# Kernel tuning notes

Measured on AMD Instinct MI355X. Metric: run time of the kernel, lower is better.

The kernel has to match this reference:

```python
import jax, jax.numpy as jnp
import numpy as np

B, D_IN, M, D_MEM = 65536, 64, 2048, 64


def setup_inputs() -> dict:
    key = jax.random.key(0)
    k = jax.random.split(key, 5)
    glorot = lambda kk, shape: jax.random.uniform(
        kk, shape, jnp.float32,
        -jnp.sqrt(6.0 / (shape[0] + shape[1])), jnp.sqrt(6.0 / (shape[0] + shape[1])))
    return {
        "inputs": jax.random.normal(k[0], (B, D_IN), jnp.float32),
        "W_att": glorot(k[1], (D_IN, M)),
        "b_att": jnp.zeros((M,), jnp.float32),
        "W_write": glorot(k[2], (D_IN, D_MEM)),
        "b_write": jnp.zeros((D_MEM,), jnp.float32),
        "memory": glorot(k[3], (M, D_MEM)),
        "update_gate": jnp.full((M,), 0.5, jnp.float32),
    }


def reference(inputs, W_att, b_att, W_write, b_write, memory, update_gate):
    # Read attention: Dense(memory_size, softmax) -> [B, M]
    read_attention = jax.nn.softmax(inputs @ W_att + b_att, axis=-1)
    # Read: [B, M] @ [M, Dm] -> [B, Dm]
    read_vector = read_attention @ memory
    # Write candidate: Dense(memory_dim, tanh) -> [B, Dm]
    candidate_write = jnp.tanh(inputs @ W_write + b_write)
    aggregated_write = jnp.mean(candidate_write, axis=0)[None, :]  # [1, Dm]
    write_attention = jnp.mean(read_attention, axis=0)             # [M]
    update_weights = (write_attention * update_gate)[:, None]      # [M, 1]
    # Gated in-place memory update (returned as new state)
    new_memory = memory * (1.0 - update_weights) + update_weights * aggregated_write
    return read_vector, new_memory
```

## Files before the change

kernel.cpp:

```cpp
#include <hip/hip_runtime.h>
#include <hip/hip_bf16.h>

typedef unsigned int   u32;
typedef unsigned short u16;

typedef __bf16 bf16x8 __attribute__((ext_vector_type(8)));
typedef float  f32x4  __attribute__((ext_vector_type(4)));
typedef u32    u32x4  __attribute__((ext_vector_type(4)));

union Frag { u32x4 u; bf16x8 b; };

#define MFMA16 __builtin_amdgcn_mfma_f32_16x16x32_bf16

#define B_ROWS 65536
#define D_IN   64
#define M_SZ   2048
#define D_MEM  64

#define WT_OFF      0
#define MEMT_OFF    262144
#define WWT_OFF     524288
#define CSF_OFF     532480
#define AGF_OFF     540672
#define CSP_OFF     540928
#define AGP_OFF     8929536
#define WS_REQUIRED 9191680

#define L2E 1.4426950408889634f

__device__ __forceinline__ float bf2f(u16 h) { return __uint_as_float(((u32)h) << 16); }
__device__ __forceinline__ u16 f2bf(float f) {
    u32 u = __float_as_uint(f);
    return (u16)((u + 0x7FFFu + ((u >> 16) & 1u)) >> 16);
}
__device__ __forceinline__ u16 f2bf_fast(float f) {
    return (u16)((__float_as_uint(f) + 0x8000u) >> 16);
}
#if defined(__has_builtin) && __has_builtin(__builtin_amdgcn_exp2f)
__device__ __forceinline__ float exp2fast(float x) { return __builtin_amdgcn_exp2f(x); }
#else
__device__ __forceinline__ float exp2fast(float x) { return __expf(x * 0.6931471805599453f); }
#endif
__device__ __forceinline__ float tanh_fast(float x) {
    const float e = exp2fast(x * (2.0f * L2E));
    return 1.0f - 2.0f * __builtin_amdgcn_rcpf(e + 1.0f);
}
__device__ __forceinline__ bool detect_bf16(const void* ug) {
    return ((const u32*)ug)[0] == 0x3F003F00u;
}
__device__ __forceinline__ float load_elem(const void* p, size_t i, bool isbf) {
    return isbf ? bf2f(((const u16*)p)[i]) : ((const float*)p)[i];
}

__global__ void __launch_bounds__(256)
prep_kernel(const void* Watt, const void* mem_in, const void* Wwr, const void* ug,
            u16* Wt, u16* memT, u16* Wwt, float* CSF)
{
    const bool isbf = detect_bf16(ug);
    const int b = blockIdx.x;
    const int t = threadIdx.x;
    if (b == 65) {
        for (int i = t; i < 2112; i += 256) CSF[i] = 0.f;
        return;
    }
    __shared__ u16 tile[64][65];
    const void* src; u16* dst; int R, C, rb, cb;
    if (b < 32)      { src = Watt;   dst = Wt;   R = 64;   C = 2048; rb = 0;           cb = b * 64; }
    else if (b < 64) { src = mem_in; dst = memT; R = 2048; C = 64;   rb = (b-32) * 64; cb = 0;      }
    else             { src = Wwr;    dst = Wwt;  R = 64;   C = 64;   rb = 0;           cb = 0;      }

#pragma unroll
    for (int j = 0; j < 16; ++j) {
        int e = j * 256 + t;
        int r = e >> 6, c = e & 63;
        float v = load_elem(src, (size_t)(rb + r) * C + cb + c, isbf);
        tile[r][c] = f2bf(v);
    }
    __syncthreads();
#pragma unroll
    for (int j = 0; j < 16; ++j) {
        int e = j * 256 + t;
        int c2 = e >> 6, r2 = e & 63;
        dst[(size_t)(cb + c2) * R + rb + r2] = tile[r2][c2];
    }
}

__global__ void __launch_bounds__(256, 2)
main_kernel(const void* x_in, const void* batt_in, const void* bwrite_in,
            const u16* __restrict__ Wt, const u16* __restrict__ memT,
            const u16* __restrict__ Wwt, const void* ug,
            float* CSF, float* AGF, u16* cs_part, u16* ag_part,
            int use_part, void* out)
{
    const bool isbf = detect_bf16(ug);
    const int tid = threadIdx.x;
    const int lane = tid & 63, wave = tid >> 6;
    const int quad = lane >> 4, l4 = lane & 15;
    const int rowbase = blockIdx.x * 128;
    const int wrow = blockIdx.x * 4 + wave;

    __shared__ __align__(16) u16 WtL[2][64][72];
    __shared__ __align__(16) u16 MeL[2][64][72];
    __shared__ __align__(16) u16 P[4][32][72];
    __shared__ float battL[2048];

    {
        const int i0 = tid * 8;
#pragma unroll
        for (int j = 0; j < 8; ++j)
            battL[i0 + j] = load_elem(batt_in, i0 + j, isbf) * L2E;
    }

    const int srow = tid >> 2, sg = (tid & 3) * 16;
    auto stageWt = [&](int c, int b) {
        const u16* g = Wt + ((size_t)c * 64 + srow) * 64 + sg;
        u32x4 v0 = *(const u32x4*)g;
        u32x4 v1 = *(const u32x4*)(g + 8);
        *(u32x4*)&WtL[b][srow][sg]     = v0;
        *(u32x4*)&WtL[b][srow][sg + 8] = v1;
    };
    auto stageMe = [&](int c, int b) {
        const u16* g = memT + (size_t)srow * 2048 + c * 64 + sg;
        u32x4 v0 = *(const u32x4*)g;
        u32x4 v1 = *(const u32x4*)(g + 8);
        *(u32x4*)&MeL[b][srow][sg]     = v0;
        *(u32x4*)&MeL[b][srow][sg + 8] = v1;
    };

    Frag a[2][2];
#pragma unroll
    for (int rg = 0; rg < 2; ++rg) {
        const int arow = rowbase + wave * 32 + rg * 16 + l4;
        if (isbf) {
            const u16* xp = (const u16*)x_in + (size_t)arow * 64 + quad * 8;
            a[rg][0].u = *(const u32x4*)xp;
            a[rg][1].u = *(const u32x4*)(xp + 32);
        } else {
            const float* xp = (const float*)x_in + (size_t)arow * 64 + quad * 8;
#pragma unroll
            for (int j = 0; j < 8; ++j) {
                ((u16*)&a[rg][0])[j] = f2bf(xp[j]);
                ((u16*)&a[rg][1])[j] = f2bf(xp[32 + j]);
            }
        }
    }
    const f32x4 zf = {0.f, 0.f, 0.f, 0.f};

    stageWt(0, 0);

    float agout = 0.f;
    {
        f32x4 accW[4][2];
#pragma unroll
        for (int t = 0; t < 4; ++t) {
            const u16* bp = Wwt + (size_t)(t * 16 + l4) * 64 + quad * 8;
            Frag b0, b1; b0.u = *(const u32x4*)bp; b1.u = *(const u32x4*)(bp + 32);
#pragma unroll
            for (int rg = 0; rg < 2; ++rg) {
                accW[t][rg] = MFMA16(a[rg][0].b, b0.b, zf, 0, 0, 0);
                accW[t][rg] = MFMA16(a[rg][1].b, b1.b, accW[t][rg], 0, 0, 0);
            }
        }
#pragma unroll
        for (int t = 0; t < 4; ++t) {
            const float bw = load_elem(bwrite_in, t * 16 + l4, isbf);
            float s = 0.f;
#pragma unroll
            for (int rg = 0; rg < 2; ++rg)
#pragma unroll
                for (int i = 0; i < 4; ++i) s += tanh_fast(accW[t][rg][i] + bw);
            s += __shfl_xor(s, 16, 64);
            s += __shfl_xor(s, 32, 64);
            if (quad == t) agout = s;
        }
    }
    if (use_part) ag_part[wrow * 64 + lane] = f2bf(agout);
    else          atomicAdd(&AGF[lane], agout);

    __syncthreads();

    float lr[2][4] = {{0.f,0.f,0.f,0.f},{0.f,0.f,0.f,0.f}};
    for (int c = 0; c < 32; ++c) {
        const int buf = c & 1;
        if (c < 31) stageWt(c + 1, buf ^ 1);
        const int mbase = c * 64;
        Frag wb0[4], wb1[4]; float bl[4];
#pragma unroll
        for (int t = 0; t < 4; ++t) {
            wb0[t].u = *(const u32x4*)&WtL[buf][t * 16 + l4][quad * 8];
            wb1[t].u = *(const u32x4*)&WtL[buf][t * 16 + l4][32 + quad * 8];
            bl[t] = battL[mbase + t * 16 + l4];
        }
#pragma unroll
        for (int t = 0; t < 4; ++t)
#pragma unroll
            for (int rg = 0; rg < 2; ++rg) {
                f32x4 acc = MFMA16(a[rg][0].b, wb0[t].b, zf, 0, 0, 0);
                acc = MFMA16(a[rg][1].b, wb1[t].b, acc, 0, 0, 0);
#pragma unroll
                for (int i = 0; i < 4; ++i)
                    lr[rg][i] += exp2fast(fmaf(acc[i], L2E, bl[t]));
            }
        __syncthreads();
    }
#pragma unroll
    for (int rg = 0; rg < 2; ++rg)
#pragma unroll
        for (int i = 0; i < 4; ++i) {
            float v = lr[rg][i];
            v += __shfl_xor(v, 1, 64); v += __shfl_xor(v, 2, 64);
            v += __shfl_xor(v, 4, 64); v += __shfl_xor(v, 8, 64);
            lr[rg][i] = 1.f / v;
        }

    f32x4 oacc[2][4] = {{zf,zf,zf,zf},{zf,zf,zf,zf}};
    stageWt(0, 0); stageMe(0, 0);
    __syncthreads();
    for (int c = 0; c < 32; ++c) {
        const int buf = c & 1;
        if (c < 31) { stageWt(c + 1, buf ^ 1); stageMe(c + 1, buf ^ 1); }
        const int mbase = c * 64;
        Frag wb0[4], wb1[4], mb0[4], mb1[4]; float bl[4];
#pragma unroll
        for (int t = 0; t < 4; ++t) {
            wb0[t].u = *(const u32x4*)&WtL[buf][t * 16 + l4][quad * 8];
            wb1[t].u = *(const u32x4*)&WtL[buf][t * 16 + l4][32 + quad * 8];
            bl[t] = battL[mbase + t * 16 + l4];
            mb0[t].u = *(const u32x4*)&MeL[buf][t * 16 + l4][quad * 8];
            mb1[t].u = *(const u32x4*)&MeL[buf][t * 16 + l4][32 + quad * 8];
        }
        float cst[4];
#pragma unroll
        for (int t = 0; t < 4; ++t) {
            float cs = 0.f;
#pragma unroll
            for (int rg = 0; rg < 2; ++rg) {
                f32x4 acc = MFMA16(a[rg][0].b, wb0[t].b, zf, 0, 0, 0);
                acc = MFMA16(a[rg][1].b, wb1[t].b, acc, 0, 0, 0);
#pragma unroll
                for (int i = 0; i < 4; ++i) {
                    const float e = exp2fast(fmaf(acc[i], L2E, bl[t]));
                    const float p = e * lr[rg][i];
                    cs += p;
                    P[wave][rg * 16 + quad * 4 + i][t * 16 + l4] = f2bf_fast(p);
                }
            }
            cst[t] = cs;
        }
        Frag ap[2][2];
#pragma unroll
        for (int rg = 0; rg < 2; ++rg) {
            ap[rg][0].u = *(const u32x4*)&P[wave][rg * 16 + l4][quad * 8];
            ap[rg][1].u = *(const u32x4*)&P[wave][rg * 16 + l4][32 + quad * 8];
        }
#pragma unroll
        for (int dt = 0; dt < 4; ++dt)
#pragma unroll
            for (int rg = 0; rg < 2; ++rg) {
                oacc[rg][dt] = MFMA16(ap[rg][0].b, mb0[dt].b, oacc[rg][dt], 0, 0, 0);
                oacc[rg][dt] = MFMA16(ap[rg][1].b, mb1[dt].b, oacc[rg][dt], 0, 0, 0);
            }
        float csout = 0.f;
#pragma unroll
        for (int t = 0; t < 4; ++t) {
            float v = cst[t];
            v += __shfl_xor(v, 16, 64);
            v += __shfl_xor(v, 32, 64);
            if (quad == t) csout = v;
        }
        if (use_part) cs_part[(size_t)wrow * 2048 + mbase + lane] = f2bf(csout);
        else          atomicAdd(&CSF[mbase + lane], csout);
        __syncthreads();
    }

#pragma unroll
    for (int rg = 0; rg < 2; ++rg)
#pragma unroll
        for (int dt = 0; dt < 4; ++dt)
#pragma unroll
            for (int i = 0; i < 4; ++i) {
                const int gr = rowbase + wave * 32 + rg * 16 + quad * 4 + i;
                const int d = dt * 16 + l4;
                const float v = oacc[rg][dt][i];
                if (isbf) ((u16*)out)[(size_t)gr * 64 + d] = f2bf(v);
                else      ((float*)out)[(size_t)gr * 64 + d] = v;
            }
}

__global__ void __launch_bounds__(256)
reduce_kernel(const u16* __restrict__ cs_part, const u16* __restrict__ ag_part,
              float* CSF, float* AGF)
{
    const int b = blockIdx.x, t = threadIdx.x;
    if (b < 64) {
        const int m = (b & 7) * 256 + t;
        const int w0 = (b >> 3) * 256;
        float s = 0.f;
        for (int k = 0; k < 256; ++k) s += bf2f(cs_part[(size_t)(w0 + k) * 2048 + m]);
        atomicAdd(&CSF[m], s);
    } else if (t < 64) {
        const int w0 = (b - 64) * 512;
        float s = 0.f;
        for (int k = 0; k < 512; ++k) s += bf2f(ag_part[(w0 + k) * 64 + t]);
        atomicAdd(&AGF[t], s);
    }
}

__global__ void __launch_bounds__(256)
finalize_kernel(const void* mem_in, const void* ug,
                const float* __restrict__ CSF, const float* __restrict__ AGF,
                void* out)
{
    const bool isbf = detect_bf16(ug);
    const int idx = blockIdx.x * 256 + threadIdx.x;
    const int m = idx >> 6, d = idx & 63;
    const float wa  = CSF[m] * (1.f / 65536.f);
    const float agg = AGF[d] * (1.f / 65536.f);
    const float uw  = wa * load_elem(ug, m, isbf);
    const float mv  = load_elem(mem_in, idx, isbf);
    const float nm  = mv * (1.f - uw) + uw * agg;
    if (isbf) ((u16*)out)[(size_t)4194304 + idx] = f2bf(nm);
    else      ((float*)out)[(size_t)4194304 + idx] = nm;
}

extern "C" void kernel_launch(void* const* d_in, const int* in_sizes, int n_in,
                              void* d_out, int out_size, void* d_ws, size_t ws_size,
                              hipStream_t stream)
{
    (void)in_sizes; (void)n_in; (void)out_size;
    const void* x    = d_in[0];
    const void* Watt = d_in[1];
    const void* batt = d_in[2];
    const void* Wwr  = d_in[3];
    const void* bwr  = d_in[4];
    const void* mem  = d_in[5];
    const void* ug   = d_in[6];

    char* ws = (char*)d_ws;
    u16*   Wt      = (u16*)(ws + WT_OFF);
    u16*   memT    = (u16*)(ws + MEMT_OFF);
    u16*   Wwt     = (u16*)(ws + WWT_OFF);
    float* CSF     = (float*)(ws + CSF_OFF);
    float* AGF     = (float*)(ws + AGF_OFF);
    u16*   cs_part = (u16*)(ws + CSP_OFF);
    u16*   ag_part = (u16*)(ws + AGP_OFF);
    const int use_part = (ws_size >= (size_t)WS_REQUIRED) ? 1 : 0;

    prep_kernel<<<66, 256, 0, stream>>>(Watt, mem, Wwr, ug, Wt, memT, Wwt, CSF);
    main_kernel<<<512, 256, 0, stream>>>(x, batt, bwr, Wt, memT, Wwt, ug,
                                         CSF, AGF, cs_part, ag_part,
                                         use_part, d_out);
    if (use_part)
        reduce_kernel<<<68, 256, 0, stream>>>(cs_part, ag_part, CSF, AGF);
    finalize_kernel<<<512, 256, 0, stream>>>(mem, ug, CSF, AGF, d_out);
}
```

Before: 203.0 us.

## Double block size to 512 threads and single-buffer staged W/memory tiles

Each block of main_kernel now handles 256 rows with 8 waves instead of 128 rows with 4, launched as 256 blocks. Every staged Wt and memT chunk is therefore shared by twice as many waves, halving global-to-LDS staging traffic per row. The double-buffered LDS tiles become single buffers loaded between two barriers, which frees LDS for more resident waves per CU but removes the overlap of staging with compute and adds a barrier per chunk. The launch_bounds hint changes to (512, 4), which may constrain register allocation.

```diff
diff --git a/kernel.cpp b/kernel.cpp
--- a/kernel.cpp
+++ b/kernel.cpp
@@ -85,7 +85,7 @@
     }
 }
 
-__global__ void __launch_bounds__(256, 2)
+__global__ void __launch_bounds__(512, 4)
 main_kernel(const void* x_in, const void* batt_in, const void* bwrite_in,
             const u16* __restrict__ Wt, const u16* __restrict__ memT,
             const u16* __restrict__ Wwt, const void* ug,
@@ -96,35 +96,25 @@
     const int tid = threadIdx.x;
     const int lane = tid & 63, wave = tid >> 6;
     const int quad = lane >> 4, l4 = lane & 15;
-    const int rowbase = blockIdx.x * 128;
-    const int wrow = blockIdx.x * 4 + wave;
-
-    __shared__ __align__(16) u16 WtL[2][64][72];
-    __shared__ __align__(16) u16 MeL[2][64][72];
-    __shared__ __align__(16) u16 P[4][32][72];
+    const int rowbase = blockIdx.x * 256;
+    const int wrow = blockIdx.x * 8 + wave;
+
+    __shared__ __align__(16) u16 WtL[64][72];
+    __shared__ __align__(16) u16 MeL[64][72];
+    __shared__ __align__(16) u16 P[8][32][72];
     __shared__ float battL[2048];
 
-    {
-        const int i0 = tid * 8;
-#pragma unroll
-        for (int j = 0; j < 8; ++j)
-            battL[i0 + j] = load_elem(batt_in, i0 + j, isbf) * L2E;
-    }
-
-    const int srow = tid >> 2, sg = (tid & 3) * 16;
-    auto stageWt = [&](int c, int b) {
+    for (int i = tid; i < 2048; i += 512)
+        battL[i] = load_elem(batt_in, i, isbf) * L2E;
+
+    const int srow = tid >> 3, sg = (tid & 7) * 8;
+    auto stageWt = [&](int c) {
         const u16* g = Wt + ((size_t)c * 64 + srow) * 64 + sg;
-        u32x4 v0 = *(const u32x4*)g;
-        u32x4 v1 = *(const u32x4*)(g + 8);
-        *(u32x4*)&WtL[b][srow][sg]     = v0;
-        *(u32x4*)&WtL[b][srow][sg + 8] = v1;
+        *(u32x4*)&WtL[srow][sg] = *(const u32x4*)g;
     };
-    auto stageMe = [&](int c, int b) {
+    auto stageMe = [&](int c) {
         const u16* g = memT + (size_t)srow * 2048 + c * 64 + sg;
-        u32x4 v0 = *(const u32x4*)g;
-        u32x4 v1 = *(const u32x4*)(g + 8);
-        *(u32x4*)&MeL[b][srow][sg]     = v0;
-        *(u32x4*)&MeL[b][srow][sg + 8] = v1;
+        *(u32x4*)&MeL[srow][sg] = *(const u32x4*)g;
     };
 
     Frag a[2][2];
@@ -146,8 +136,6 @@
     }
     const f32x4 zf = {0.f, 0.f, 0.f, 0.f};
 
-    stageWt(0, 0);
-
     float agout = 0.f;
     {
         f32x4 accW[4][2];
@@ -177,18 +165,17 @@
     if (use_part) ag_part[wrow * 64 + lane] = f2bf(agout);
     else          atomicAdd(&AGF[lane], agout);
 
-    __syncthreads();
-
     float lr[2][4] = {{0.f,0.f,0.f,0.f},{0.f,0.f,0.f,0.f}};
     for (int c = 0; c < 32; ++c) {
-        const int buf = c & 1;
-        if (c < 31) stageWt(c + 1, buf ^ 1);
+        __syncthreads();
+        stageWt(c);
+        __syncthreads();
         const int mbase = c * 64;
         Frag wb0[4], wb1[4]; float bl[4];
 #pragma unroll
         for (int t = 0; t < 4; ++t) {
-            wb0[t].u = *(const u32x4*)&WtL[buf][t * 16 + l4][quad * 8];
-            wb1[t].u = *(const u32x4*)&WtL[buf][t * 16 + l4][32 + quad * 8];
+            wb0[t].u = *(const u32x4*)&WtL[t * 16 + l4][quad * 8];
+            wb1[t].u = *(const u32x4*)&WtL[t * 16 + l4][32 + quad * 8];
             bl[t] = battL[mbase + t * 16 + l4];
         }
 #pragma unroll
@@ -201,7 +188,6 @@
                 for (int i = 0; i < 4; ++i)
                     lr[rg][i] += exp2fast(fmaf(acc[i], L2E, bl[t]));
             }
-        __syncthreads();
     }
 #pragma unroll
     for (int rg = 0; rg < 2; ++rg)
@@ -214,20 +200,19 @@
         }
 
     f32x4 oacc[2][4] = {{zf,zf,zf,zf},{zf,zf,zf,zf}};
-    stageWt(0, 0); stageMe(0, 0);
-    __syncthreads();
     for (int c = 0; c < 32; ++c) {
-        const int buf = c & 1;
-        if (c < 31) { stageWt(c + 1, buf ^ 1); stageMe(c + 1, buf ^ 1); }
+        __syncthreads();
+        stageWt(c); stageMe(c);
+        __syncthreads();
         const int mbase = c * 64;
         Frag wb0[4], wb1[4], mb0[4], mb1[4]; float bl[4];
 #pragma unroll
         for (int t = 0; t < 4; ++t) {
-            wb0[t].u = *(const u32x4*)&WtL[buf][t * 16 + l4][quad * 8];
-            wb1[t].u = *(const u32x4*)&WtL[buf][t * 16 + l4][32 + quad * 8];
+            wb0[t].u = *(const u32x4*)&WtL[t * 16 + l4][quad * 8];
+            wb1[t].u = *(const u32x4*)&WtL[t * 16 + l4][32 + quad * 8];
             bl[t] = battL[mbase + t * 16 + l4];
-            mb0[t].u = *(const u32x4*)&MeL[buf][t * 16 + l4][quad * 8];
-            mb1[t].u = *(const u32x4*)&MeL[buf][t * 16 + l4][32 + quad * 8];
+            mb0[t].u = *(const u32x4*)&MeL[t * 16 + l4][quad * 8];
+            mb1[t].u = *(const u32x4*)&MeL[t * 16 + l4][32 + quad * 8];
         }
         float cst[4];
 #pragma unroll
@@ -270,7 +255,6 @@
         }
         if (use_part) cs_part[(size_t)wrow * 2048 + mbase + lane] = f2bf(csout);
         else          atomicAdd(&CSF[mbase + lane], csout);
-        __syncthreads();
     }
 
 #pragma unroll
@@ -347,7 +331,7 @@
     const int use_part = (ws_size >= (size_t)WS_REQUIRED) ? 1 : 0;
 
     prep_kernel<<<66, 256, 0, stream>>>(Watt, mem, Wwr, ug, Wt, memT, Wwt, CSF);
-    main_kernel<<<512, 256, 0, stream>>>(x, batt, bwr, Wt, memT, Wwt, ug,
+    main_kernel<<<256, 512, 0, stream>>>(x, batt, bwr, Wt, memT, Wwt, ug,
                                          CSF, AGF, cs_part, ag_part,
                                          use_part, d_out);
     if (use_part)
```

After: 213.2 us. 1.05x slower.

## Shrink LDS footprint and raise occupancy to three blocks per CU

Applied to the files above, without the earlier changes.

Drops the 8KB shared bias table and reads the attention bias straight from global memory inside the loops. Halves the per-wave probability staging buffer by handling the two row groups one after another, reusing a 16-row P tile. Raises launch bounds to 3 blocks per SM to hide latency. The cost is extra global loads of bias per chunk, a tighter register budget that may cause spills, and more serialisation between the exp and MFMA phases.

```diff
diff --git a/kernel.cpp b/kernel.cpp
--- a/kernel.cpp
+++ b/kernel.cpp
@@ -85,7 +85,7 @@
     }
 }
 
-__global__ void __launch_bounds__(256, 2)
+__global__ void __launch_bounds__(256, 3)
 main_kernel(const void* x_in, const void* batt_in, const void* bwrite_in,
             const u16* __restrict__ Wt, const u16* __restrict__ memT,
             const u16* __restrict__ Wwt, const void* ug,
@@ -101,15 +101,7 @@
 
     __shared__ __align__(16) u16 WtL[2][64][72];
     __shared__ __align__(16) u16 MeL[2][64][72];
-    __shared__ __align__(16) u16 P[4][32][72];
-    __shared__ float battL[2048];
-
-    {
-        const int i0 = tid * 8;
-#pragma unroll
-        for (int j = 0; j < 8; ++j)
-            battL[i0 + j] = load_elem(batt_in, i0 + j, isbf) * L2E;
-    }
+    __shared__ __align__(16) u16 P[4][16][72];
 
     const int srow = tid >> 2, sg = (tid & 3) * 16;
     auto stageWt = [&](int c, int b) {
@@ -189,7 +181,7 @@
         for (int t = 0; t < 4; ++t) {
             wb0[t].u = *(const u32x4*)&WtL[buf][t * 16 + l4][quad * 8];
             wb1[t].u = *(const u32x4*)&WtL[buf][t * 16 + l4][32 + quad * 8];
-            bl[t] = battL[mbase + t * 16 + l4];
+            bl[t] = load_elem(batt_in, mbase + t * 16 + l4, isbf) * L2E;
         }
 #pragma unroll
         for (int t = 0; t < 4; ++t)
@@ -225,41 +217,36 @@
         for (int t = 0; t < 4; ++t) {
             wb0[t].u = *(const u32x4*)&WtL[buf][t * 16 + l4][quad * 8];
             wb1[t].u = *(const u32x4*)&WtL[buf][t * 16 + l4][32 + quad * 8];
-            bl[t] = battL[mbase + t * 16 + l4];
+            bl[t] = load_elem(batt_in, mbase + t * 16 + l4, isbf) * L2E;
             mb0[t].u = *(const u32x4*)&MeL[buf][t * 16 + l4][quad * 8];
             mb1[t].u = *(const u32x4*)&MeL[buf][t * 16 + l4][32 + quad * 8];
         }
-        float cst[4];
-#pragma unroll
-        for (int t = 0; t < 4; ++t) {
-            float cs = 0.f;
-#pragma unroll
-            for (int rg = 0; rg < 2; ++rg) {
+        float cst[4] = {0.f, 0.f, 0.f, 0.f};
+#pragma unroll
+        for (int rg = 0; rg < 2; ++rg) {
+#pragma unroll
+            for (int t = 0; t < 4; ++t) {
                 f32x4 acc = MFMA16(a[rg][0].b, wb0[t].b, zf, 0, 0, 0);
                 acc = MFMA16(a[rg][1].b, wb1[t].b, acc, 0, 0, 0);
+                float cs = 0.f;
 #pragma unroll
                 for (int i = 0; i < 4; ++i) {
                     const float e = exp2fast(fmaf(acc[i], L2E, bl[t]));
                     const float p = e * lr[rg][i];
                     cs += p;
-                    P[wave][rg * 16 + quad * 4 + i][t * 16 + l4] = f2bf_fast(p);
+                    P[wave][quad * 4 + i][t * 16 + l4] = f2bf_fast(p);
                 }
-            }
-            cst[t] = cs;
-        }
-        Frag ap[2][2];
-#pragma unroll
-        for (int rg = 0; rg < 2; ++rg) {
-            ap[rg][0].u = *(const u32x4*)&P[wave][rg * 16 + l4][quad * 8];
-            ap[rg][1].u = *(const u32x4*)&P[wave][rg * 16 + l4][32 + quad * 8];
-        }
-#pragma unroll
-        for (int dt = 0; dt < 4; ++dt)
-#pragma unroll
-            for (int rg = 0; rg < 2; ++rg) {
-                oacc[rg][dt] = MFMA16(ap[rg][0].b, mb0[dt].b, oacc[rg][dt], 0, 0, 0);
-                oacc[rg][dt] = MFMA16(ap[rg][1].b, mb1[dt].b, oacc[rg][dt], 0, 0, 0);
-            }
+                cst[t] += cs;
+            }
+            Frag ap0, ap1;
+            ap0.u = *(const u32x4*)&P[wave][l4][quad * 8];
+            ap1.u = *(const u32x4*)&P[wave][l4][32 + quad * 8];
+#pragma unroll
+            for (int dt = 0; dt < 4; ++dt) {
+                oacc[rg][dt] = MFMA16(ap0.b, mb0[dt].b, oacc[rg][dt], 0, 0, 0);
+                oacc[rg][dt] = MFMA16(ap1.b, mb1[dt].b, oacc[rg][dt], 0, 0, 0);
+            }
+        }
         float csout = 0.f;
 #pragma unroll
         for (int t = 0; t < 4; ++t) {
```

Result: slower. 209.9 us (+3.4%).
